# Kernel optimization log

Measured on AMD Instinct MI355X. Metric: run time of the kernel, lower is better.

Reference implementation:

```python
import jax, jax.numpy as jnp
import numpy as np

HEADS, HEAD_SIZE, FREQS, MAX_PERIOD = 16, 64, 256, 10000
D_MODEL = 1024
NEG_INF = -1e9


def sinusoid_embedding(seq_len, frequencies, max_period):
    # Interleaved sin/cos sinusoid table, shape (seq_len, frequencies).
    pos = np.arange(seq_len, dtype=np.float64)[:, None]
    idx = np.arange(frequencies)[None, :]
    inv_freq = max_period ** (-(idx // 2 * 2) / frequencies)
    angle = pos * inv_freq
    table = np.where(idx % 2 == 0, np.sin(angle), np.cos(angle))
    return table.astype(np.float32)


def relative_causal(scores):
    # scores: (b, n, q, v) with v indexing relative distance d = q - k.
    # Returns a[..., q, k] = scores[..., q, q - k] (k > q entries are masked later).
    L = scores.shape[-1]
    d = jnp.clip(jnp.arange(L)[:, None] - jnp.arange(L)[None, :], 0, L - 1)  # (q, k)
    return jnp.take_along_axis(scores, d[None, None, :, :], axis=-1)


def setup_inputs() -> dict:
    key = jax.random.key(0)
    ks = jax.random.split(key, 4)
    u = np.sqrt(3.0)
    inp = jax.random.normal(ks[0], (2, 2048, D_MODEL), dtype=jnp.float32)
    qkv = jax.random.uniform(ks[1], (D_MODEL, 3, HEADS, HEAD_SIZE), jnp.float32, -u, u)
    q_bias = jnp.zeros((HEADS, HEAD_SIZE), jnp.float32)
    positional = jax.random.uniform(ks[2], (FREQS, HEADS, HEAD_SIZE), jnp.float32, -u, u)
    out_kernel = jax.random.uniform(ks[3], (HEADS * HEAD_SIZE, D_MODEL), jnp.float32, -u, u)
    out_bias = jnp.zeros((D_MODEL,), jnp.float32)
    return {"input": inp, "qkv": qkv, "q_bias": q_bias, "positional": positional,
            "out_kernel": out_kernel, "out_bias": out_bias}


def reference(input, qkv, q_bias, positional, out_kernel, out_bias):
    b, s, x = input.shape
    n, h = HEADS, HEAD_SIZE
    # QKV projection with unit-scaling forward factor.
    w = qkv * (3.0 * x * h * n) ** -0.25
    q, k, v = jnp.einsum('bsx,xAnh->Abnsh', input, w)  # each (b, n, s, h)
    q = q + q_bias[:, None, :]
    # Content scores.
    a = jnp.einsum('bnqh,bnkh->bnqk', q, k) * h ** -0.5
    # Relative-positional scores (Transformer-XL style).
    sins = jnp.asarray(np.sqrt(2.0) * sinusoid_embedding(s, FREQS, MAX_PERIOD))
    emb = jnp.einsum('sf,fnh->nsh', sins, positional * FREQS ** -0.5)
    pos_scores = jnp.einsum('bnqh,nvh->bnqv', q, emb) * h ** -0.5
    a = a + relative_causal(pos_scores)
    # Causal mask + softmax.
    mask = jnp.tril(jnp.ones((s, s), dtype=bool))
    a = jax.nn.softmax(jnp.where(mask, a, NEG_INF), axis=-1)
    # Weighted sum and output projection (Dense, scale_for='both').
    o = jnp.einsum('bnqk,bnkh->bqnh', a, v).reshape(b, s, n * h)
    fan_in, fan_out = out_kernel.shape
    out = o @ (out_kernel * (fan_in * fan_out) ** -0.25) + out_bias
    return out
```

## Files before the change

kernel.cpp:

```cpp
#include <hip/hip_runtime.h>
#include <math.h>

#define BATCH 2
#define SEQ 2048
#define DMODEL 1024
#define HEADS 16
#define HSIZE 64
#define FREQS 256
#define NH 1024
#define QKVN 3072

typedef __bf16 bf16;
typedef __bf16 bf16x8 __attribute__((ext_vector_type(8)));
typedef float f32x4 __attribute__((ext_vector_type(4)));

static __device__ __forceinline__ unsigned short bf16_bits(float v) {
    bf16 b = (bf16)v; return __builtin_bit_cast(unsigned short, b);
}

static __device__ __forceinline__ void gload16(const void* g, void* l) {
    __builtin_amdgcn_global_load_lds(
        (const __attribute__((address_space(1))) unsigned int*)g,
        (__attribute__((address_space(3))) unsigned int*)l, 16, 0, 0);
}

__global__ __launch_bounds__(256) void prep_kernel(
    const float* __restrict__ inp, const float* __restrict__ qkv_w,
    const float* __restrict__ out_kernel, const float* __restrict__ positional,
    bf16* __restrict__ a_bf, bf16* __restrict__ wt_qkv,
    bf16* __restrict__ wt_out, bf16* __restrict__ wt_pos,
    bf16* __restrict__ sins_bf)
{
    __shared__ float tile[32][33];
    const int id = blockIdx.x, t = threadIdx.x;

    if (id < 4096) {
        int i = id * 256 + t;
        float4 v = ((const float4*)inp)[i];
        ushort4 o;
        o.x = bf16_bits(v.x); o.y = bf16_bits(v.y);
        o.z = bf16_bits(v.z); o.w = bf16_bits(v.w);
        ((ushort4*)a_bf)[i] = o;
        return;
    }
    if (id < 6144) {
        int i = (id - 4096) * 256 + t;
        int s = i >> 8, f = i & 255;
        double e = -(double)((f >> 1) << 1) / (double)FREQS;
        double invf = pow(10000.0, e);
        double ang = (double)s * invf;
        double v = (f & 1) ? cos(ang) : sin(ang);
        sins_bf[i] = (bf16)(float)(1.4142135623730951 * v);
        return;
    }
    int id2 = id - 6144;
    const float* src; bf16* dst; int R, C, c0, r0;
    if (id2 < 3072) {
        src = qkv_w; dst = wt_qkv; R = 1024; C = 3072;
        c0 = (id2 % 96) * 32; r0 = (id2 / 96) * 32;
    } else if (id2 < 4096) {
        id2 -= 3072;
        src = out_kernel; dst = wt_out; R = 1024; C = 1024;
        c0 = (id2 & 31) * 32; r0 = (id2 >> 5) * 32;
    } else {
        id2 -= 4096;
        src = positional; dst = wt_pos; R = 256; C = 1024;
        c0 = (id2 & 31) * 32; r0 = (id2 >> 5) * 32;
    }
    const int tx = t & 31, ty = t >> 5;
#pragma unroll
    for (int i = 0; i < 4; i++)
        tile[ty + i * 8][tx] = src[(size_t)(r0 + ty + i * 8) * C + c0 + tx];
    __syncthreads();
#pragma unroll
    for (int i = 0; i < 4; i++)
        dst[(size_t)(c0 + ty + i * 8) * R + r0 + tx] = (bf16)tile[tx][ty + i * 8];
}

template<int EPI>
__global__ __launch_bounds__(256) void mfma_gemm(
    const bf16* __restrict__ A, const bf16* __restrict__ Bt,
    int K, float alpha, const float* __restrict__ bias,
    float* __restrict__ outf, bf16* __restrict__ ob0, bf16* __restrict__ ob1,
    bf16* __restrict__ ob2,
    const bf16* __restrict__ A2, const bf16* __restrict__ Bt2,
    bf16* __restrict__ ob3, float alpha2)
{
    __shared__ __align__(16) bf16 Atile[2][128 * 32];
    __shared__ __align__(16) bf16 Btile[2][128 * 32];

    const int t    = threadIdx.x;
    const int lane = t & 63;
    const int w    = t >> 6;
    const int quad = lane >> 4;
    const int l16  = lane & 15;
    const int wm   = (w >> 1) * 64;
    const int wn   = (w & 1) * 64;

    bool embp = false;
    int m0 = blockIdx.y * 128, n0 = blockIdx.x * 128, Kl = K;
    const bf16* Ap = A; const bf16* Btp = Bt; float al = alpha;
    if constexpr (EPI == 1) {
        if (blockIdx.x >= 24) {
            if (blockIdx.y >= 16) return;
            embp = true;
            n0 = (blockIdx.x - 24) * 128;
            Kl = FREQS; Ap = A2; Btp = Bt2; al = alpha2;
        }
    }
    const bool swapv = (EPI == 1) && !embp && (n0 >= 2048);

    const int rS = t >> 2;
    const int cS = (t & 3) ^ ((rS >> 1) & 3);
    const bf16* ag0 = Ap  + (size_t)(m0 + rS) * Kl + cS * 8;
    const bf16* ag1 = ag0 + (size_t)64 * Kl;
    const bf16* bg0 = Btp + (size_t)(n0 + rS) * Kl + cS * 8;
    const bf16* bg1 = bg0 + (size_t)64 * Kl;

    int aoff[4], boff[4];
#pragma unroll
    for (int mi = 0; mi < 4; ++mi) {
        int r = wm + mi * 16 + l16;
        aoff[mi] = r * 32 + ((quad ^ ((r >> 1) & 3)) * 8);
    }
#pragma unroll
    for (int ni = 0; ni < 4; ++ni) {
        int r = wn + ni * 16 + l16;
        boff[ni] = r * 32 + ((quad ^ ((r >> 1) & 3)) * 8);
    }

    gload16(ag0, (char*)Atile[0] + t * 16);
    gload16(ag1, (char*)Atile[0] + 4096 + t * 16);
    gload16(bg0, (char*)Btile[0] + t * 16);
    gload16(bg1, (char*)Btile[0] + 4096 + t * 16);

    const int nK = Kl >> 5;
    f32x4 acc[4][4] = {};

    for (int kk = 0; kk < nK; ++kk) {
        __syncthreads();
        if (kk + 1 < nK) {
            ag0 += 32; ag1 += 32; bg0 += 32; bg1 += 32;
            char* ad = (char*)Atile[(kk + 1) & 1];
            char* bd = (char*)Btile[(kk + 1) & 1];
            gload16(ag0, ad + t * 16); gload16(ag1, ad + 4096 + t * 16);
            gload16(bg0, bd + t * 16); gload16(bg1, bd + 4096 + t * 16);
        }
        const bf16* ab = Atile[kk & 1];
        const bf16* bb = Btile[kk & 1];
        bf16x8 af[4], bfr[4];
#pragma unroll
        for (int mi = 0; mi < 4; ++mi) af[mi] = *(const bf16x8*)(ab + aoff[mi]);
#pragma unroll
        for (int ni = 0; ni < 4; ++ni) bfr[ni] = *(const bf16x8*)(bb + boff[ni]);

        if (!swapv) {
#pragma unroll
            for (int mi = 0; mi < 4; ++mi)
#pragma unroll
                for (int ni = 0; ni < 4; ++ni)
                    acc[mi][ni] = __builtin_amdgcn_mfma_f32_16x16x32_bf16(
                        af[mi], bfr[ni], acc[mi][ni], 0, 0, 0);
        } else {
#pragma unroll
            for (int mi = 0; mi < 4; ++mi)
#pragma unroll
                for (int ni = 0; ni < 4; ++ni)
                    acc[mi][ni] = __builtin_amdgcn_mfma_f32_16x16x32_bf16(
                        bfr[ni], af[mi], acc[mi][ni], 0, 0, 0);
        }
    }

    if constexpr (EPI == 0) {
#pragma unroll
        for (int mi = 0; mi < 4; ++mi)
#pragma unroll
            for (int ni = 0; ni < 4; ++ni) {
                int col = n0 + wn + ni * 16 + l16;
                float bb = bias[col];
#pragma unroll
                for (int rg = 0; rg < 4; ++rg) {
                    int row = m0 + wm + mi * 16 + quad * 4 + rg;
                    outf[(size_t)row * NH + col] = acc[mi][ni][rg] * al + bb;
                }
            }
    } else {
        if (embp) {
#pragma unroll
            for (int mi = 0; mi < 4; ++mi)
#pragma unroll
                for (int ni = 0; ni < 4; ++ni) {
                    int col = n0 + wn + ni * 16 + l16;
                    int head = col >> 6, h = col & 63;
#pragma unroll
                    for (int rg = 0; rg < 4; ++rg) {
                        int d = m0 + wm + mi * 16 + quad * 4 + rg;
                        int hs = h ^ (((d + 63) & 7) << 3);
                        ob3[((size_t)(head * SEQ + d)) * 64 + hs] =
                            (bf16)(acc[mi][ni][rg] * al);
                    }
                }
        } else if (n0 >= 2048) {
#pragma unroll
            for (int mi = 0; mi < 4; ++mi)
#pragma unroll
                for (int ni = 0; ni < 4; ++ni) {
                    int mcol = m0 + wm + mi * 16 + l16;
                    int bb = mcol >> 11, s = mcol & 2047;
#pragma unroll
                    for (int rg = 0; rg < 4; ++rg) {
                        int hg = n0 + wn + ni * 16 + quad * 4 + rg;
                        int head = (hg & 1023) >> 6, h = hg & 63;
                        int ss = s ^ ((h & 7) << 3);
                        ob2[((size_t)((bb * 16 + head) * 64 + h)) * SEQ + ss] =
                            (bf16)(acc[mi][ni][rg] * al);
                    }
                }
        } else {
            const int whichk = (n0 >= 1024);
#pragma unroll
            for (int mi = 0; mi < 4; ++mi)
#pragma unroll
                for (int ni = 0; ni < 4; ++ni) {
                    int cg   = (n0 + wn + ni * 16 + l16) & 1023;
                    int head = cg >> 6, h = cg & 63;
                    float qbv = whichk ? 0.0f : bias[cg];
#pragma unroll
                    for (int rg = 0; rg < 4; ++rg) {
                        int row = m0 + wm + mi * 16 + quad * 4 + rg;
                        int bb = row >> 11, s = row & 2047;
                        float v = acc[mi][ni][rg] * al;
                        if (whichk) {
                            int hs = h ^ ((s & 7) << 3);
                            ob1[((size_t)((bb * 16 + head) * SEQ + s)) * 64 + hs] = (bf16)v;
                        } else {
                            ob0[((size_t)((bb * 16 + head) * SEQ + s)) * 64 + h] =
                                (bf16)((v + qbv) * 0.125f);
                        }
                    }
                }
        }
    }
}

__global__ __launch_bounds__(256, 2) void attn_kernel(
    const bf16* __restrict__ Qb, const bf16* __restrict__ Kb,
    const bf16* __restrict__ Vtb, const bf16* __restrict__ Eb,
    bf16* __restrict__ o)
{
    __shared__ __align__(16) bf16 Ks[2][4096];
    __shared__ __align__(16) bf16 Vts[2][4096];
    __shared__ __align__(16) bf16 Es[256 * 64];
    __shared__ __align__(16) bf16 PS[4][16][72];

    const int t    = threadIdx.x;
    const int lane = t & 63;
    const int w    = t >> 6;
    const int quad = lane >> 4;
    const int l16  = lane & 15;

    const int bx = blockIdx.x;
    const int b  = bx >> 4, n = bx & 15;
    const int yy = blockIdx.y;
    const int qc = (yy < 8) ? (15 - 2 * yy) : (2 * yy - 16);
    const int q0 = qc * 128;
    const int KT = 2 * qc + 2;
    const int qw0 = q0 + 16 * w;
    const int qw1 = qw0 + 64;

    const bf16* __restrict__ Qp = Qb  + (size_t)bx * SEQ * 64;
    const bf16* __restrict__ Kp = Kb  + (size_t)bx * SEQ * 64;
    const bf16* __restrict__ Vp = Vtb + (size_t)bx * SEQ * 64;
    const bf16* __restrict__ Ep = Eb  + (size_t)n  * SEQ * 64;

    const int key8 = (l16 & 7) << 3;
    const int ec0  = ((quad * 8) ^ key8) * 2;
    const int ec1  = ((32 + quad * 8) ^ key8) * 2;

    bf16x8 qf[2][2];
    qf[0][0] = *(const bf16x8*)(Qp + (size_t)(qw0 + l16) * 64 + quad * 8);
    qf[0][1] = *(const bf16x8*)(Qp + (size_t)(qw0 + l16) * 64 + 32 + quad * 8);
    qf[1][0] = *(const bf16x8*)(Qp + (size_t)(qw1 + l16) * 64 + quad * 8);
    qf[1][1] = *(const bf16x8*)(Qp + (size_t)(qw1 + l16) * 64 + 32 + quad * 8);

    int dsta[4];
    bool condp[4];
#pragma unroll
    for (int rg = 0; rg < 4; ++rg) {
        int rr   = quad * 4 + rg;
        int l16c = (rr + 15 - l16) & 15;
        dsta[rg]  = ((lane & 48) + l16c) << 2;
        condp[rg] = rr > l16c;
    }

    f32x4 O[2][4] = {};
    float lsum[2][4] = {};

    {
        gload16(Kp + t * 8,        (char*)Ks[0] + t * 16);
        gload16(Kp + 2048 + t * 8, (char*)Ks[0] + 4096 + t * 16);
        gload16(Vp + (size_t)(t >> 3) * SEQ + (t & 7) * 8,        (char*)Vts[0] + t * 16);
        gload16(Vp + (size_t)((t >> 3) + 32) * SEQ + (t & 7) * 8, (char*)Vts[0] + 4096 + t * 16);
        const long D0 = (long)q0 - 63;
#pragma unroll
        for (int g = 0; g < 6; ++g)
            gload16(Ep + (D0 + 32 * g) * 64 + t * 8, (char*)Es + g * 4096 + t * 16);
    }

    auto load_kv = [&](const char* kb, const char* vb,
                       bf16x8 (&kf)[4][2], bf16x8 (&vf)[4][2]) {
#pragma unroll
        for (int j = 0; j < 4; ++j) {
            const char* kp = kb + (j * 16 + l16) * 128;
            kf[j][0] = *(const bf16x8*)(kp + ec0);
            kf[j][1] = *(const bf16x8*)(kp + ec1);
            const char* vp = vb + (j * 16 + l16) * 128;
            vf[j][0] = *(const bf16x8*)(vp + ec0);
            vf[j][1] = *(const bf16x8*)(vp + ec1);
        }
    };
    auto eread = [&](int rb, bf16x8 (&ef)[5][2]) {
#pragma unroll
        for (int jj = 0; jj < 5; ++jj) {
            const char* ep = (const char*)Es + ((rb + 16 * jj + l16) & 255) * 128;
            ef[jj][0] = *(const bf16x8*)(ep + ec0);
            ef[jj][1] = *(const bf16x8*)(ep + ec1);
        }
    };
    auto qkmfma = [&](const bf16x8 (&q2)[2], const bf16x8 (&kf)[4][2],
                      f32x4 (&S)[4]) {
#pragma unroll
        for (int j = 0; j < 4; ++j) {
            f32x4 a = {0, 0, 0, 0};
            a = __builtin_amdgcn_mfma_f32_16x16x32_bf16(q2[1], kf[j][1], a, 0, 0, 0);
            a = __builtin_amdgcn_mfma_f32_16x16x32_bf16(q2[0], kf[j][0], a, 0, 0, 0);
            S[j] = a;
        }
    };
    auto pamfma = [&](const bf16x8 (&q2)[2], const bf16x8 (&ef)[5][2],
                      f32x4 (&pa)[5]) {
#pragma unroll
        for (int jj = 0; jj < 5; ++jj) {
            f32x4 a = {0, 0, 0, 0};
            a = __builtin_amdgcn_mfma_f32_16x16x32_bf16(q2[1], ef[jj][1], a, 0, 0, 0);
            a = __builtin_amdgcn_mfma_f32_16x16x32_bf16(q2[0], ef[jj][0], a, 0, 0, 0);
            pa[jj] = a;
        }
    };
    auto smax = [&](int kq, f32x4 (&S)[4], const f32x4 (&pa)[5], float (&ls)[4]) {
#pragma unroll
        for (int j = 0; j < 4; ++j) {
#pragma unroll
            for (int rg = 0; rg < 4; ++rg) {
                float vsel = condp[rg] ? pa[4 - j][rg] : pa[3 - j][rg];
                int pv = __builtin_amdgcn_ds_permute(dsta[rg], __float_as_int(vsel));
                float sv = S[j][rg] + __int_as_float(pv);
                bool valid = (j * 16 + l16) <= (kq + quad * 4 + rg);
                S[j][rg] = valid ? __expf(sv) : 0.0f;
            }
        }
#pragma unroll
        for (int rg = 0; rg < 4; ++rg)
            ls[rg] += S[0][rg] + S[1][rg] + S[2][rg] + S[3][rg];
    };
    auto ps_write = [&](const f32x4 (&S)[4]) {
#pragma unroll
        for (int j = 0; j < 4; ++j)
#pragma unroll
            for (int rg = 0; rg < 4; ++rg)
                PS[w][quad * 4 + rg][j * 16 + l16] = (bf16)S[j][rg];
    };
    auto pvmfma = [&](const bf16x8 (&vf)[4][2], f32x4 (&Oc)[4]) {
        bf16x8 pf0 = *(const bf16x8*)(&PS[w][l16][quad * 8]);
        bf16x8 pf1 = *(const bf16x8*)(&PS[w][l16][32 + quad * 8]);
#pragma unroll
        for (int j4 = 0; j4 < 4; ++j4) {
            Oc[j4] = __builtin_amdgcn_mfma_f32_16x16x32_bf16(pf1, vf[j4][1], Oc[j4], 0, 0, 0);
            Oc[j4] = __builtin_amdgcn_mfma_f32_16x16x32_bf16(pf0, vf[j4][0], Oc[j4], 0, 0, 0);
        }
    };

    for (int kt = 0; kt < KT - 1; ++kt) {
        const int k0 = kt * 64;
        __syncthreads();

        {
            const int nt = kt + 1;
            bf16* kd = Ks[nt & 1];
            bf16* vd = Vts[nt & 1];
            const bf16* ksrc = Kp + nt * 4096;
            gload16(ksrc + t * 8,        (char*)kd + t * 16);
            gload16(ksrc + 2048 + t * 8, (char*)kd + 4096 + t * 16);
            gload16(Vp + (size_t)(t >> 3) * SEQ + nt * 64 + (t & 7) * 8,
                    (char*)vd + t * 16);
            gload16(Vp + (size_t)((t >> 3) + 32) * SEQ + nt * 64 + (t & 7) * 8,
                    (char*)vd + 4096 + t * 16);
            const long d0 = (long)q0 - nt * 64 - 63;
            const int rI = (-64 * nt) & 255;
            gload16(Ep + d0 * 64 + t * 8,        (char*)Es + rI * 128 + t * 16);
            gload16(Ep + (d0 + 32) * 64 + t * 8, (char*)Es + rI * 128 + 4096 + t * 16);
        }

        bf16x8 kf[4][2], vf[4][2];
        load_kv((const char*)Ks[kt & 1], (const char*)Vts[kt & 1], kf, vf);

        bf16x8 ef0[5][2];
        eread(16 * w - k0, ef0);
        f32x4 S0[4], pa0[5];
        __builtin_amdgcn_s_setprio(1);
        qkmfma(qf[0], kf, S0);
        pamfma(qf[0], ef0, pa0);
        __builtin_amdgcn_s_setprio(0);
        smax(qw0 - k0, S0, pa0, lsum[0]);

        bf16x8 ef1[5][2];
        eread(16 * w + 64 - k0, ef1);
        ps_write(S0);

        f32x4 S1[4], pa1[5];
        __builtin_amdgcn_s_setprio(1);
        qkmfma(qf[1], kf, S1);
        pamfma(qf[1], ef1, pa1);
        pvmfma(vf, O[0]);
        __builtin_amdgcn_s_setprio(0);

        smax(qw1 - k0, S1, pa1, lsum[1]);
        ps_write(S1);
        __builtin_amdgcn_s_setprio(1);
        pvmfma(vf, O[1]);
        __builtin_amdgcn_s_setprio(0);
    }

    {
        const int kt = KT - 1, k0 = kt * 64;
        __syncthreads();
        bf16x8 kf[4][2], vf[4][2];
        load_kv((const char*)Ks[kt & 1], (const char*)Vts[kt & 1], kf, vf);
        bf16x8 ef1[5][2];
        eread(16 * w + 64 - k0, ef1);
        f32x4 S1[4], pa1[5];
        qkmfma(qf[1], kf, S1);
        pamfma(qf[1], ef1, pa1);
        smax(qw1 - k0, S1, pa1, lsum[1]);
        ps_write(S1);
        pvmfma(vf, O[1]);
    }

#pragma unroll
    for (int c = 0; c < 2; ++c) {
#pragma unroll
        for (int rg = 0; rg < 4; ++rg) {
            float s = lsum[c][rg];
            s += __shfl_xor(s, 1);
            s += __shfl_xor(s, 2);
            s += __shfl_xor(s, 4);
            s += __shfl_xor(s, 8);
            float inv = 1.0f / s;
            int q = (c ? qw1 : qw0) + quad * 4 + rg;
            size_t ro = ((size_t)(b * SEQ + q)) * NH + n * 64;
            o[ro +  0 + l16] = (bf16)(O[c][0][rg] * inv);
            o[ro + 16 + l16] = (bf16)(O[c][1][rg] * inv);
            o[ro + 32 + l16] = (bf16)(O[c][2][rg] * inv);
            o[ro + 48 + l16] = (bf16)(O[c][3][rg] * inv);
        }
    }
}

extern "C" void kernel_launch(void* const* d_in, const int* in_sizes, int n_in,
                              void* d_out, int out_size, void* d_ws, size_t ws_size,
                              hipStream_t stream) {
    const float* inp        = (const float*)d_in[0];
    const float* qkv_w      = (const float*)d_in[1];
    const float* q_bias     = (const float*)d_in[2];
    const float* positional = (const float*)d_in[3];
    const float* out_kernel = (const float*)d_in[4];
    const float* out_bias   = (const float*)d_in[5];

    char* p = (char*)d_ws;
    auto alloc = [&](size_t bytes) {
        char* q = p; p += (bytes + 255) & ~(size_t)255; return q;
    };
    bf16* qbuf    = (bf16*)alloc((size_t)BATCH * HEADS * SEQ * HSIZE * 2);
    bf16* kbuf    = (bf16*)alloc((size_t)BATCH * HEADS * SEQ * HSIZE * 2);
    bf16* vtbuf   = (bf16*)alloc((size_t)BATCH * HEADS * SEQ * HSIZE * 2);
    bf16* embT    = (bf16*)alloc((size_t)HEADS * SEQ * HSIZE * 2);
    bf16* sins_bf = (bf16*)alloc((size_t)SEQ * FREQS * 2);
    bf16* obuf    = (bf16*)alloc((size_t)BATCH * SEQ * NH * 2);
    bf16* a_bf    = (bf16*)alloc((size_t)BATCH * SEQ * DMODEL * 2);
    bf16* wt_qkv  = (bf16*)alloc((size_t)QKVN * DMODEL * 2);
    bf16* wt_out  = (bf16*)alloc((size_t)NH * DMODEL * 2);
    bf16* wt_pos  = (bf16*)alloc((size_t)NH * FREQS * 2);

    const float qkv_scale = (float)pow(3.0 * DMODEL * HSIZE * HEADS, -0.25);
    const float emb_scale = 0.0625f;
    const float out_scale = 0.03125f;

    prep_kernel<<<10496, 256, 0, stream>>>(
        inp, qkv_w, out_kernel, positional, a_bf, wt_qkv, wt_out, wt_pos, sins_bf);

    mfma_gemm<1><<<dim3(32, 32), 256, 0, stream>>>(
        a_bf, wt_qkv, DMODEL, qkv_scale, q_bias, nullptr, qbuf, kbuf, vtbuf,
        sins_bf, wt_pos, embT, emb_scale);

    attn_kernel<<<dim3(32, 16), 256, 0, stream>>>(
        qbuf, kbuf, vtbuf, embT, obuf);

    mfma_gemm<0><<<dim3(8, 32), 256, 0, stream>>>(
        obuf, wt_out, DMODEL, out_scale, out_bias, (float*)d_out,
        nullptr, nullptr, nullptr, nullptr, nullptr, nullptr, 0.0f);
}
```

Before: 263.6 us.

## Split long causal query chunks across two blocks with partial-softmax merge

The eight longest query chunks (qc 8-15) are split in two along the key dimension, so the attention grid grows from 16 to 24 blocks per head and per-block work is better balanced. Each half writes unnormalized fp32 output and row sums into reused workspace (aliasing the a_bf/wt_pos buffers), and a new merge kernel sums the halves, normalizes, and writes bf16. The softmax has no running max, so the partial results can simply be added. This adds an extra launch, fp32 partial traffic, and a workspace reshuffle that relies on those buffers being dead after the QKV GEMM.

```diff
diff --git a/kernel.cpp b/kernel.cpp
--- a/kernel.cpp
+++ b/kernel.cpp
@@ -243,10 +243,15 @@
     }
 }
 
+__device__ const unsigned char YQC[24]  = {15,15,7,14,14,13,13,6,12,12,11,11,
+                                           5,10,10,9,9,4,8,8,3,2,1,0};
+__device__ const unsigned char YPRT[24] = {0,1,2,0,1,0,1,2,0,1,0,1,
+                                           2,0,1,0,1,2,0,1,2,2,2,2};
+
 __global__ __launch_bounds__(256, 2) void attn_kernel(
     const bf16* __restrict__ Qb, const bf16* __restrict__ Kb,
     const bf16* __restrict__ Vtb, const bf16* __restrict__ Eb,
-    bf16* __restrict__ o)
+    bf16* __restrict__ o, float* __restrict__ Opart, float* __restrict__ Lpart)
 {
     __shared__ __align__(16) bf16 Ks[2][4096];
     __shared__ __align__(16) bf16 Vts[2][4096];
@@ -262,9 +267,14 @@
     const int bx = blockIdx.x;
     const int b  = bx >> 4, n = bx & 15;
     const int yy = blockIdx.y;
-    const int qc = (yy < 8) ? (15 - 2 * yy) : (2 * yy - 16);
+    const int qc = YQC[yy];
+    const int pr = YPRT[yy];
     const int q0 = qc * 128;
     const int KT = 2 * qc + 2;
+    const int kt0 = (pr == 1) ? (qc + 1) : 0;
+    const int kt1 = (pr == 0) ? (qc + 1) : KT;
+    const bool haspeel = (pr != 0);
+    const bool split   = (pr != 2);
     const int qw0 = q0 + 16 * w;
     const int qw1 = qw0 + 64;
 
@@ -297,14 +307,20 @@
     float lsum[2][4] = {};
 
     {
-        gload16(Kp + t * 8,        (char*)Ks[0] + t * 16);
-        gload16(Kp + 2048 + t * 8, (char*)Ks[0] + 4096 + t * 16);
-        gload16(Vp + (size_t)(t >> 3) * SEQ + (t & 7) * 8,        (char*)Vts[0] + t * 16);
-        gload16(Vp + (size_t)((t >> 3) + 32) * SEQ + (t & 7) * 8, (char*)Vts[0] + 4096 + t * 16);
-        const long D0 = (long)q0 - 63;
-#pragma unroll
-        for (int g = 0; g < 6; ++g)
-            gload16(Ep + (D0 + 32 * g) * 64 + t * 8, (char*)Es + g * 4096 + t * 16);
+        const bf16* ksrc = Kp + kt0 * 4096;
+        char* kd = (char*)Ks[kt0 & 1];
+        char* vd = (char*)Vts[kt0 & 1];
+        gload16(ksrc + t * 8,        kd + t * 16);
+        gload16(ksrc + 2048 + t * 8, kd + 4096 + t * 16);
+        gload16(Vp + (size_t)(t >> 3) * SEQ + kt0 * 64 + (t & 7) * 8,        vd + t * 16);
+        gload16(Vp + (size_t)((t >> 3) + 32) * SEQ + kt0 * 64 + (t & 7) * 8, vd + 4096 + t * 16);
+        const long D0 = (long)q0 - 64 * kt0 - 63;
+        const int rI0 = (-64 * kt0) & 255;
+#pragma unroll
+        for (int g = 0; g < 6; ++g) {
+            const int sI = (rI0 + 32 * g) & 255;
+            gload16(Ep + (D0 + 32 * g) * 64 + t * 8, (char*)Es + sI * 128 + t * 16);
+        }
     }
 
     auto load_kv = [&](const char* kb, const char* vb,
@@ -380,12 +396,13 @@
         }
     };
 
-    for (int kt = 0; kt < KT - 1; ++kt) {
+    const int ktE = kt1 - (haspeel ? 1 : 0);
+    for (int kt = kt0; kt < ktE; ++kt) {
         const int k0 = kt * 64;
         __syncthreads();
 
-        {
-            const int nt = kt + 1;
+        const int nt = kt + 1;
+        if (nt < kt1) {
             bf16* kd = Ks[nt & 1];
             bf16* vd = Vts[nt & 1];
             const bf16* ksrc = Kp + nt * 4096;
@@ -431,8 +448,8 @@
         __builtin_amdgcn_s_setprio(0);
     }
 
-    {
-        const int kt = KT - 1, k0 = kt * 64;
+    if (haspeel) {
+        const int kt = kt1 - 1, k0 = kt * 64;
         __syncthreads();
         bf16x8 kf[4][2], vf[4][2];
         load_kv((const char*)Ks[kt & 1], (const char*)Vts[kt & 1], kf, vf);
@@ -446,24 +463,72 @@
         pvmfma(vf, O[1]);
     }
 
-#pragma unroll
-    for (int c = 0; c < 2; ++c) {
-#pragma unroll
-        for (int rg = 0; rg < 4; ++rg) {
-            float s = lsum[c][rg];
-            s += __shfl_xor(s, 1);
-            s += __shfl_xor(s, 2);
-            s += __shfl_xor(s, 4);
-            s += __shfl_xor(s, 8);
-            float inv = 1.0f / s;
-            int q = (c ? qw1 : qw0) + quad * 4 + rg;
-            size_t ro = ((size_t)(b * SEQ + q)) * NH + n * 64;
-            o[ro +  0 + l16] = (bf16)(O[c][0][rg] * inv);
-            o[ro + 16 + l16] = (bf16)(O[c][1][rg] * inv);
-            o[ro + 32 + l16] = (bf16)(O[c][2][rg] * inv);
-            o[ro + 48 + l16] = (bf16)(O[c][3][rg] * inv);
-        }
-    }
+    if (!split) {
+#pragma unroll
+        for (int c = 0; c < 2; ++c) {
+#pragma unroll
+            for (int rg = 0; rg < 4; ++rg) {
+                float s = lsum[c][rg];
+                s += __shfl_xor(s, 1);
+                s += __shfl_xor(s, 2);
+                s += __shfl_xor(s, 4);
+                s += __shfl_xor(s, 8);
+                float inv = 1.0f / s;
+                int q = (c ? qw1 : qw0) + quad * 4 + rg;
+                size_t ro = ((size_t)(b * SEQ + q)) * NH + n * 64;
+                o[ro +  0 + l16] = (bf16)(O[c][0][rg] * inv);
+                o[ro + 16 + l16] = (bf16)(O[c][1][rg] * inv);
+                o[ro + 32 + l16] = (bf16)(O[c][2][rg] * inv);
+                o[ro + 48 + l16] = (bf16)(O[c][3][rg] * inv);
+            }
+        }
+    } else {
+        const int pslot = pr;
+        float* Ob = Opart + ((size_t)(pslot * 32 + bx)) * 1024 * 64;
+        float* Lb = Lpart + ((size_t)(pslot * 32 + bx)) * 1024;
+#pragma unroll
+        for (int c = 0; c < 2; ++c) {
+#pragma unroll
+            for (int rg = 0; rg < 4; ++rg) {
+                float s = lsum[c][rg];
+                s += __shfl_xor(s, 1);
+                s += __shfl_xor(s, 2);
+                s += __shfl_xor(s, 4);
+                s += __shfl_xor(s, 8);
+                int q = (c ? qw1 : qw0) + quad * 4 + rg;
+                int rloc = q - 1024;
+                size_t ro = (size_t)rloc * 64;
+                Ob[ro +  0 + l16] = O[c][0][rg];
+                Ob[ro + 16 + l16] = O[c][1][rg];
+                Ob[ro + 32 + l16] = O[c][2][rg];
+                Ob[ro + 48 + l16] = O[c][3][rg];
+                if (l16 == 0) Lb[rloc] = s;
+            }
+        }
+    }
+}
+
+__global__ __launch_bounds__(256) void merge_kernel(
+    const float* __restrict__ Opart, const float* __restrict__ Lpart,
+    bf16* __restrict__ o)
+{
+    int idx = blockIdx.x * 256 + threadIdx.x;
+    int h4 = idx & 15;
+    int r  = (idx >> 4) & 1023;
+    int bx = idx >> 14;
+    size_t i0 = (((size_t)bx        * 1024 + r) * 64 + h4 * 4);
+    size_t i1 = (((size_t)(32 + bx) * 1024 + r) * 64 + h4 * 4);
+    float4 a = *(const float4*)(Opart + i0);
+    float4 c = *(const float4*)(Opart + i1);
+    float inv = 1.0f / (Lpart[bx * 1024 + r] + Lpart[32 * 1024 + bx * 1024 + r]);
+    int b = bx >> 4, n = bx & 15;
+    size_t ro = ((size_t)(b * SEQ + 1024 + r)) * NH + n * 64 + h4 * 4;
+    ushort4 wv;
+    wv.x = bf16_bits((a.x + c.x) * inv);
+    wv.y = bf16_bits((a.y + c.y) * inv);
+    wv.z = bf16_bits((a.z + c.z) * inv);
+    wv.w = bf16_bits((a.w + c.w) * inv);
+    *(ushort4*)(o + ro) = wv;
 }
 
 extern "C" void kernel_launch(void* const* d_in, const int* in_sizes, int n_in,
@@ -486,10 +551,13 @@
     bf16* embT    = (bf16*)alloc((size_t)HEADS * SEQ * HSIZE * 2);
     bf16* sins_bf = (bf16*)alloc((size_t)SEQ * FREQS * 2);
     bf16* obuf    = (bf16*)alloc((size_t)BATCH * SEQ * NH * 2);
+    bf16* wt_out  = (bf16*)alloc((size_t)NH * DMODEL * 2);
+    bf16* wt_pos  = (bf16*)alloc((size_t)NH * FREQS * 2);
     bf16* a_bf    = (bf16*)alloc((size_t)BATCH * SEQ * DMODEL * 2);
     bf16* wt_qkv  = (bf16*)alloc((size_t)QKVN * DMODEL * 2);
-    bf16* wt_out  = (bf16*)alloc((size_t)NH * DMODEL * 2);
-    bf16* wt_pos  = (bf16*)alloc((size_t)NH * FREQS * 2);
+    (void)       alloc((size_t)2097152);
+    float* Opart  = (float*)a_bf;
+    float* Lpart  = (float*)wt_pos;
 
     const float qkv_scale = (float)pow(3.0 * DMODEL * HSIZE * HEADS, -0.25);
     const float emb_scale = 0.0625f;
@@ -502,8 +570,10 @@
         a_bf, wt_qkv, DMODEL, qkv_scale, q_bias, nullptr, qbuf, kbuf, vtbuf,
         sins_bf, wt_pos, embT, emb_scale);
 
-    attn_kernel<<<dim3(32, 16), 256, 0, stream>>>(
-        qbuf, kbuf, vtbuf, embT, obuf);
+    attn_kernel<<<dim3(32, 24), 256, 0, stream>>>(
+        qbuf, kbuf, vtbuf, embT, obuf, Opart, Lpart);
+
+    merge_kernel<<<2048, 256, 0, stream>>>(Opart, Lpart, obuf);
 
     mfma_gemm<0><<<dim3(8, 32), 256, 0, stream>>>(
         obuf, wt_out, DMODEL, out_scale, out_bias, (float*)d_out,
```

New measurement: 259.1 us. No clear change (-1.7%).
